# Performance work log

Hardware: AMD Instinct MI355X
Metric: run time of the kernel (lower is better)

The kernel has to match this reference:

```python
import jax, jax.numpy as jnp
import numpy as np

L, B, S, D, H, DK, F = 6, 4, 2048, 512, 8, 64, 2048


def setup_inputs() -> dict:
    key = jax.random.key(0)
    ks = iter(jax.random.split(key, 40))
    def rn(shape, scale=0.02):
        return jax.random.normal(next(ks), shape, jnp.float32) * scale
    inp = {
        "x": jax.random.normal(next(ks), (B, S, D), jnp.float32),
        "enc": jax.random.normal(next(ks), (B, S, D), jnp.float32),
    }
    for pre in ("sa", "ca"):
        inp[f"{pre}_wq"] = rn((L, D, H * DK)); inp[f"{pre}_bq"] = jnp.zeros((L, H * DK), jnp.float32)
        inp[f"{pre}_wk"] = rn((L, D, H * DK)); inp[f"{pre}_bk"] = jnp.zeros((L, H * DK), jnp.float32)
        inp[f"{pre}_wv"] = rn((L, D, H * DK)); inp[f"{pre}_bv"] = jnp.zeros((L, H * DK), jnp.float32)
        inp[f"{pre}_wo"] = rn((L, H * DK, D)); inp[f"{pre}_bo"] = jnp.zeros((L, D), jnp.float32)
    for i in (1, 2, 3):
        inp[f"ln{i}_g"] = jnp.ones((L, D), jnp.float32)
        inp[f"ln{i}_b"] = jnp.zeros((L, D), jnp.float32)
    inp["ff_w1"] = rn((L, D, F)); inp["ff_b1"] = jnp.zeros((L, F), jnp.float32)
    inp["ff_w2"] = rn((L, F, D)); inp["ff_b2"] = jnp.zeros((L, D), jnp.float32)
    return inp


def _layer_norm(z, g, b, eps=1e-5):
    m = z.mean(-1, keepdims=True)
    v = z.var(-1, keepdims=True)
    return (z - m) * jax.lax.rsqrt(v + eps) * g + b


def _mha(q_in, kv_in, wq, bq, wk, bk, wv, bv, wo, bo, causal_bias):
    b, s, _ = q_in.shape
    Q = (q_in @ wq + bq).reshape(b, s, H, DK)   # [B,S,H,DK]
    K = (kv_in @ wk + bk).reshape(b, s, H, DK)
    V = (kv_in @ wv + bv).reshape(b, s, H, DK)
    scores = jnp.einsum("bqhd,bkhd->bhqk", Q, K) / jnp.float32(DK) ** 0.5
    if causal_bias is not None:
        scores = scores + causal_bias  # additive -inf above diagonal
    w = jax.nn.softmax(scores, axis=-1)
    att = jnp.einsum("bhqk,bkhd->bqhd", w, V).reshape(b, s, H * DK)
    return att @ wo + bo


def reference(x, enc, sa_wq, sa_bq, sa_wk, sa_bk, sa_wv, sa_bv, sa_wo, sa_bo,
              ca_wq, ca_bq, ca_wk, ca_bk, ca_wv, ca_bv, ca_wo, ca_bo,
              ln1_g, ln1_b, ln2_g, ln2_b, ln3_g, ln3_b,
              ff_w1, ff_b1, ff_w2, ff_b2):
    s = x.shape[1]
    causal_bias = jnp.triu(jnp.full((s, s), -jnp.inf, jnp.float32), 1)

    params = (sa_wq, sa_bq, sa_wk, sa_bk, sa_wv, sa_bv, sa_wo, sa_bo,
              ca_wq, ca_bq, ca_wk, ca_bk, ca_wv, ca_bv, ca_wo, ca_bo,
              ln1_g, ln1_b, ln2_g, ln2_b, ln3_g, ln3_b,
              ff_w1, ff_b1, ff_w2, ff_b2)

    def block(h, p):
        (swq, sbq, swk, sbk, swv, sbv, swo, sbo,
         cwq, cbq, cwk, cbk, cwv, cbv, cwo, cbo,
         g1, b1, g2, b2, g3, b3, w1, bb1, w2, bb2) = p
        # masked self-attention + residual + LN  (faithful to source)
        x1 = _layer_norm(h + _mha(h, h, swq, sbq, swk, sbk, swv, sbv, swo, sbo, causal_bias), g1, b1)
        # cross-attention; residual comes from the BLOCK INPUT h (source bug kept)
        y = _layer_norm(h + _mha(x1, enc, cwq, cbq, cwk, cbk, cwv, cbv, cwo, cbo, None), g2, b2)
        # FFN; residual from x1 (source bug kept)
        out = _layer_norm(x1 + (jax.nn.relu(y @ w1 + bb1) @ w2 + bb2), g3, b3)
        return out, None

    out, _ = jax.lax.scan(block, x, params)
    return out
```

## Files before the change

kernel.cpp:

```cpp
#include <hip/hip_runtime.h>
#include <stdint.h>

#define LCOUNT 6
#define BB 4
#define SS 2048
#define DD 512
#define HH 8
#define DKK 64
#define FFDIM 2048
#define MM (BB*SS)

typedef __attribute__((ext_vector_type(8))) __bf16 bf16x8;
typedef __attribute__((ext_vector_type(4))) float f32x4;
typedef unsigned short u16;

__device__ __forceinline__ u16 f2bf(float f) {
  union { __bf16 h; u16 u; } v; v.h = (__bf16)f; return v.u;
}
__device__ __forceinline__ float bf2f(u16 u) {
  union { uint32_t u; float f; } v; v.u = ((uint32_t)u) << 16;
  return v.f;
}

__device__ __forceinline__ void gload_lds16(const u16* gsrc, u16* ldst) {
  __builtin_amdgcn_global_load_lds((const __attribute__((address_space(1))) char*)gsrc,
                                   (__attribute__((address_space(3))) char*)ldst, 16, 0, 0);
}

__global__ __launch_bounds__(256)
void prep(const float* __restrict__ x, const float* __restrict__ enc,
          u16* __restrict__ Hb, u16* __restrict__ Eb,
          const float* a0, const float* a1, const float* a2,
          const float* c0, const float* c1, const float* c2,
          float* dqkv, float* dca) {
  if (blockIdx.x < 4096) {
    int i = (blockIdx.x * 256 + threadIdx.x) * 8;
    const int half = MM * 512;
    const float* src = (i < half) ? x : enc;
    u16* dst = (i < half) ? Hb : Eb;
    int j = (i < half) ? i : i - half;
    float4 a = *(const float4*)&src[j];
    float4 b = *(const float4*)&src[j + 4];
    union { u16 us[8]; uint4 v; } pk;
    pk.us[0] = f2bf(a.x); pk.us[1] = f2bf(a.y); pk.us[2] = f2bf(a.z); pk.us[3] = f2bf(a.w);
    pk.us[4] = f2bf(b.x); pk.us[5] = f2bf(b.y); pk.us[6] = f2bf(b.z); pk.us[7] = f2bf(b.w);
    *(uint4*)&dst[j] = pk.v;
  } else {
    int i = (blockIdx.x - 4096) * 256 + threadIdx.x;
    const int half = LCOUNT * 1536;
    if (i >= 2 * half) return;
    bool ca = i >= half;
    int j = ca ? i - half : i;
    int l = j / 1536, cc = j % 1536;
    const float* s = cc < 512 ? (ca ? c0 : a0) : cc < 1024 ? (ca ? c1 : a1) : (ca ? c2 : a2);
    (ca ? dca : dqkv)[j] = s[l * 512 + (cc & 511)];
  }
}

struct WtBatch {
  const float* src[8];
  u16* dst[8];
  unsigned long long lstr[8];
};
__global__ __launch_bounds__(256) void wtrans8(WtBatch wb) {
  __shared__ float tile[64 * 65];
  const int z = blockIdx.z;
  const int slot = z / 6, l = z - slot * 6;
  const float* Wl = wb.src[slot] + (size_t)l * 512 * 512;
  u16* Wtl = wb.dst[slot] + (size_t)l * wb.lstr[slot];
  const int n0 = blockIdx.x * 64, k0 = blockIdx.y * 64;
  const int tid = threadIdx.x;
  const int r = tid >> 2, c4 = (tid & 3) * 16;
#pragma unroll
  for (int j = 0; j < 16; j += 4) {
    float4 v = *(const float4*)&Wl[(size_t)(k0 + r) * 512 + n0 + c4 + j];
    tile[r * 65 + c4 + j + 0] = v.x;
    tile[r * 65 + c4 + j + 1] = v.y;
    tile[r * 65 + c4 + j + 2] = v.z;
    tile[r * 65 + c4 + j + 3] = v.w;
  }
  __syncthreads();
  const int nr = tid >> 2, kc = (tid & 3) * 16;
#pragma unroll
  for (int half = 0; half < 2; ++half) {
    union { u16 us[8]; uint4 v; } pk;
#pragma unroll
    for (int e = 0; e < 8; ++e) pk.us[e] = f2bf(tile[(kc + half * 8 + e) * 65 + nr]);
    *(uint4*)&Wtl[(size_t)(n0 + nr) * 512 + k0 + kc + half * 8] = pk.v;
  }
}

__global__ __launch_bounds__(256)
void wtrans_ffn(const float* __restrict__ w1, const float* __restrict__ w2,
                u16* __restrict__ w1t, u16* __restrict__ w2t) {
  __shared__ float tile[64 * 65];
  const int z = blockIdx.y;
  const bool is2 = z >= 6;
  const int l = is2 ? z - 6 : z;
  const float* Wl = (is2 ? w2 : w1) + (size_t)l * 512 * 2048;
  u16* Wtl = (is2 ? w2t : w1t) + (size_t)l * 512 * 2048;
  const int K_ = is2 ? 2048 : 512, N_ = is2 ? 512 : 2048;
  const int bx = blockIdx.x;
  const int n0 = is2 ? (bx & 7) * 64 : (bx & 31) * 64;
  const int k0 = is2 ? (bx >> 3) * 64 : (bx >> 5) * 64;
  const int tid = threadIdx.x;
  const int r = tid >> 2, c4 = (tid & 3) * 16;
#pragma unroll
  for (int j = 0; j < 16; j += 4) {
    float4 v = *(const float4*)&Wl[(size_t)(k0 + r) * N_ + n0 + c4 + j];
    tile[r * 65 + c4 + j + 0] = v.x;
    tile[r * 65 + c4 + j + 1] = v.y;
    tile[r * 65 + c4 + j + 2] = v.z;
    tile[r * 65 + c4 + j + 3] = v.w;
  }
  __syncthreads();
  const int nr = tid >> 2, kc = (tid & 3) * 16;
#pragma unroll
  for (int half = 0; half < 2; ++half) {
    union { u16 us[8]; uint4 v; } pk;
#pragma unroll
    for (int e = 0; e < 8; ++e) pk.us[e] = f2bf(tile[(kc + half * 8 + e) * 65 + nr]);
    *(uint4*)&Wtl[(size_t)(n0 + nr) * K_ + k0 + kc + half * 8] = pk.v;
  }
}

template <int BMT, int BNT, int BKT, bool RELU, bool VT, bool RES>
__global__ __launch_bounds__(256)
void gemm_bt(const u16* __restrict__ A, const u16* __restrict__ Bt,
             const float* __restrict__ bias, u16* __restrict__ C,
             int N_, int K_, int CS, u16* __restrict__ vt, int vtc0,
             const u16* __restrict__ A2, int a2col,
             const u16* __restrict__ resid) {
  constexpr int MR = BMT / 32;
  constexpr int NR = BNT / 32;
  constexpr int CH = BKT / 8;
  constexpr int RPR = 2048 / BKT;
  constexpr int KS = BKT / 32;
  __shared__ u16 As[BMT * BKT];
  __shared__ u16 Bs[BNT * BKT];
  const int tid = threadIdx.x;
  const int wid = tid >> 6, lane = tid & 63;
  const int l15 = lane & 15, g = lane >> 4;
  const int wr = wid >> 1, wc = wid & 1;
  const int lrow = (CH == 8) ? (lane >> 3) : (lane >> 4);
  const int lch  = lane & (CH - 1);
  const int wrows = 64 / CH;
  const int lin = blockIdx.x + gridDim.x * blockIdx.y;
  const int nwg = gridDim.x * gridDim.y;
  const int swz = (lin & 7) * (nwg >> 3) + (lin >> 3);
  const int brow = (swz / gridDim.x) * BMT;
  const int bcol = (swz % gridDim.x) * BNT;
  const u16* Ap = (A2 != nullptr && bcol >= a2col) ? A2 : A;

  f32x4 acc[MR][NR];
#pragma unroll
  for (int m = 0; m < MR; ++m)
#pragma unroll
    for (int n = 0; n < NR; ++n) acc[m][n] = (f32x4){0.f, 0.f, 0.f, 0.f};

  for (int kt = 0; kt < K_; kt += BKT) {
#pragma unroll
    for (int r = 0; r < BMT / RPR; ++r) {
      int row = r * RPR + wid * wrows + lrow;
      int slot = lch ^ (row & 7);
      gload_lds16(Ap + (size_t)(brow + row) * K_ + kt + slot * 8,
                  &As[r * 2048 + wid * 512]);
    }
#pragma unroll
    for (int r = 0; r < BNT / RPR; ++r) {
      int row = r * RPR + wid * wrows + lrow;
      int slot = lch ^ (row & 7);
      gload_lds16(Bt + (size_t)(bcol + row) * K_ + kt + slot * 8,
                  &Bs[r * 2048 + wid * 512]);
    }
    __syncthreads();
#pragma unroll
    for (int ks = 0; ks < KS; ++ks) {
      bf16x8 af[MR], bfr[NR];
#pragma unroll
      for (int m = 0; m < MR; ++m) {
        int row = wr * (BMT / 2) + m * 16 + l15;
        int slot = (ks * 4 + g) ^ (row & 7);
        af[m] = *(const bf16x8*)&As[row * BKT + slot * 8];
      }
#pragma unroll
      for (int n = 0; n < NR; ++n) {
        int row = wc * (BNT / 2) + n * 16 + l15;
        int slot = (ks * 4 + g) ^ (row & 7);
        bfr[n] = *(const bf16x8*)&Bs[row * BKT + slot * 8];
      }
#pragma unroll
      for (int m = 0; m < MR; ++m)
#pragma unroll
        for (int n = 0; n < NR; ++n)
          acc[m][n] = __builtin_amdgcn_mfma_f32_16x16x32_bf16(af[m], bfr[n], acc[m][n], 0, 0, 0);
    }
    __syncthreads();
  }
#pragma unroll
  for (int n = 0; n < NR; ++n) {
    int col = bcol + wc * (BNT / 2) + n * 16 + l15;
    float bv = bias ? bias[col] : 0.f;
    if (VT && col >= vtc0) {
      int hh = (col - vtc0) >> 6, dd = (col - vtc0) & 63;
#pragma unroll
      for (int m = 0; m < MR; ++m) {
        int s0g = brow + wr * (BMT / 2) + m * 16 + g * 4;
        int bb = s0g >> 11, ss = s0g & (SS - 1);
        union { u16 us[4]; uint2 v; } pk;
#pragma unroll
        for (int r = 0; r < 4; ++r) pk.us[r] = f2bf(acc[m][n][r] + bv);
        *(uint2*)&vt[(((size_t)(bb * HH + hh)) * DKK + dd) * SS + ss] = pk.v;
      }
    } else {
#pragma unroll
      for (int m = 0; m < MR; ++m) {
#pragma unroll
        for (int r = 0; r < 4; ++r) {
          int rowg = brow + wr * (BMT / 2) + m * 16 + g * 4 + r;
          float v = acc[m][n][r] + bv;
          if (RES) v += bf2f(resid[(size_t)rowg * DD + col]);
          if (RELU) v = fmaxf(v, 0.f);
          C[(size_t)rowg * CS + col] = f2bf(v);
        }
      }
    }
  }
}

__global__ __launch_bounds__(256)
void gemm_ln(const u16* __restrict__ A, const u16* __restrict__ Bt,
             const float* __restrict__ bias, const u16* __restrict__ Res,
             const float* __restrict__ gamma, const float* __restrict__ beta,
             u16* __restrict__ Out, float* __restrict__ Ofp, int K_) {
  __shared__ u16 As[16 * 64];
  __shared__ u16 Bs[512 * 64];
  __shared__ float red[4][16][2];
  const int tid = threadIdx.x;
  const int wid = tid >> 6, lane = tid & 63;
  const int l15 = lane & 15, g = lane >> 4;
  const int lin = blockIdx.x;
  const int swz = (lin & 7) * (gridDim.x >> 3) + (lin >> 3);
  const int brow = swz * 16;
  const int lrow8 = lane >> 3, lch = lane & 7;

  f32x4 acc[8];
#pragma unroll
  for (int n = 0; n < 8; ++n) acc[n] = (f32x4){0.f, 0.f, 0.f, 0.f};

  for (int kt = 0; kt < K_; kt += 64) {
#pragma unroll
    for (int r = 0; r < 17; ++r) {
      int u = wid + 4 * r;
      if (u < 66) {
        if (u < 2) {
          int row = u * 8 + lrow8;
          int slot = lch ^ (row & 7);
          gload_lds16(A + (size_t)(brow + row) * K_ + kt + slot * 8, &As[u * 512]);
        } else {
          int row = (u - 2) * 8 + lrow8;
          int slot = lch ^ (row & 7);
          gload_lds16(Bt + (size_t)row * K_ + kt + slot * 8, &Bs[(u - 2) * 512]);
        }
      }
    }
    __syncthreads();
#pragma unroll
    for (int ks = 0; ks < 2; ++ks) {
      bf16x8 af = *(const bf16x8*)&As[l15 * 64 + (((ks * 4 + g) ^ (l15 & 7)) * 8)];
#pragma unroll
      for (int n = 0; n < 8; ++n) {
        int c = wid * 128 + n * 16 + l15;
        bf16x8 bfr = *(const bf16x8*)&Bs[c * 64 + (((ks * 4 + g) ^ (c & 7)) * 8)];
        acc[n] = __builtin_amdgcn_mfma_f32_16x16x32_bf16(af, bfr, acc[n], 0, 0, 0);
      }
    }
    __syncthreads();
  }
#pragma unroll
  for (int rd = 0; rd < 4; ++rd) {
    int off = rd * 2048 + tid * 8;
    int row = off >> 9, col = off & 511;
    uint4 v = *(const uint4*)&Res[(size_t)(brow + row) * DD + col];
    *(uint4*)&Bs[row * 520 + col] = v;
  }
  __syncthreads();
  float z[8][4];
  float s[4] = {0.f, 0.f, 0.f, 0.f}, s2[4] = {0.f, 0.f, 0.f, 0.f};
#pragma unroll
  for (int n = 0; n < 8; ++n) {
    int col = wid * 128 + n * 16 + l15;
    float bv = bias[col];
#pragma unroll
    for (int r = 0; r < 4; ++r) {
      int rl = g * 4 + r;
      float x = acc[n][r] + bv + bf2f(Bs[rl * 520 + col]);
      z[n][r] = x; s[r] += x; s2[r] += x * x;
    }
  }
#pragma unroll
  for (int r = 0; r < 4; ++r) {
    s[r] += __shfl_xor(s[r], 1);  s2[r] += __shfl_xor(s2[r], 1);
    s[r] += __shfl_xor(s[r], 2);  s2[r] += __shfl_xor(s2[r], 2);
    s[r] += __shfl_xor(s[r], 4);  s2[r] += __shfl_xor(s2[r], 4);
    s[r] += __shfl_xor(s[r], 8);  s2[r] += __shfl_xor(s2[r], 8);
  }
  if (l15 == 0) {
#pragma unroll
    for (int r = 0; r < 4; ++r) {
      red[wid][g * 4 + r][0] = s[r];
      red[wid][g * 4 + r][1] = s2[r];
    }
  }
  __syncthreads();
  float mean[4], rs[4];
#pragma unroll
  for (int r = 0; r < 4; ++r) {
    int rl = g * 4 + r;
    float ts  = red[0][rl][0] + red[1][rl][0] + red[2][rl][0] + red[3][rl][0];
    float ts2 = red[0][rl][1] + red[1][rl][1] + red[2][rl][1] + red[3][rl][1];
    float mn = ts * (1.f / 512.f);
    float var = ts2 * (1.f / 512.f) - mn * mn;
    mean[r] = mn; rs[r] = rsqrtf(var + 1e-5f);
  }
#pragma unroll
  for (int n = 0; n < 8; ++n) {
    int col = wid * 128 + n * 16 + l15;
    float gm = gamma[col], bt = beta[col];
#pragma unroll
    for (int r = 0; r < 4; ++r) {
      int rowg = brow + g * 4 + r;
      float o = (z[n][r] - mean[r]) * rs[r] * gm + bt;
      Out[(size_t)rowg * DD + col] = f2bf(o);
      if (Ofp) Ofp[(size_t)rowg * DD + col] = o;
    }
  }
}

__global__ __launch_bounds__(256)
void ln_kernel(const u16* __restrict__ A,
               const float* __restrict__ gamma, const float* __restrict__ beta,
               u16* __restrict__ out_bf, float* __restrict__ out_f32) {
  const int row = blockIdx.x * 4 + (threadIdx.x >> 6);
  const int lane = threadIdx.x & 63;
  uint4 av = *(const uint4*)&A[(size_t)row * DD + lane * 8];
  const u16* au = (const u16*)&av;
  float z[8], s = 0.f, s2 = 0.f;
#pragma unroll
  for (int j = 0; j < 8; ++j) {
    float x = bf2f(au[j]);
    z[j] = x; s += x; s2 += x * x;
  }
#pragma unroll
  for (int off = 1; off < 64; off <<= 1) {
    s += __shfl_xor(s, off);
    s2 += __shfl_xor(s2, off);
  }
  float mean = s * (1.f / 512.f);
  float var = s2 * (1.f / 512.f) - mean * mean;
  float rs = rsqrtf(var + 1e-5f);
  union { u16 us[8]; uint4 v; } pk;
#pragma unroll
  for (int j = 0; j < 8; ++j) {
    float o = (z[j] - mean) * rs * gamma[lane * 8 + j] + beta[lane * 8 + j];
    pk.us[j] = f2bf(o);
    if (out_f32) out_f32[(size_t)row * DD + lane * 8 + j] = o;
  }
  *(uint4*)&out_bf[(size_t)row * DD + lane * 8] = pk.v;
}

template <bool CAUSAL>
__global__ __launch_bounds__(256, 4)
void attn_kernel(const u16* __restrict__ Qm, const u16* __restrict__ Km,
                 const u16* __restrict__ Vt, u16* __restrict__ Om, int qks) {
  __shared__ u16 Ks[2][64 * 64];
  __shared__ u16 Vs[2][64 * 64];
  __shared__ u16 Ps[4][16 * 64];
  const int lin = blockIdx.x;
  const int bh = (lin & 7) * 4 + ((lin >> 3) >> 5);
  const int qc = (lin >> 3) & 31;
  const int qb = (qc & 1) ? (31 - (qc >> 1)) : (qc >> 1);
  const int h = bh & 7, b = bh >> 3;
  const int tid = threadIdx.x, wid = tid >> 6, lane = tid & 63;
  const int l15 = lane & 15, g = lane >> 4;
  const int qstart = qb * 64;
  const size_t qbase = ((size_t)b * SS) * qks + h * DKK;
  const size_t vtbase = (size_t)(b * HH + h) * DKK * SS;
  const size_t obase = ((size_t)b * SS) * DD + h * DKK;
  u16* psw = &Ps[wid][0];
  const int srow = wid * 8 + (lane >> 3);
  const int sslot = lane & 7;
  const int qg = qstart + wid * 16 + l15;
  const int pswz = (l15 & 7) << 1;
  const float SC = 0.18033688f;

  const u16* kp = Km + qbase;
  const u16* vp = Vt + vtbase;

  bf16x8 qf[2];
#pragma unroll
  for (int ks = 0; ks < 2; ++ks)
    qf[ks] = *(const bf16x8*)&Qm[qbase + (size_t)qg * qks + ks * 32 + g * 8];

  f32x4 oacc[4];
#pragma unroll
  for (int nb = 0; nb < 4; ++nb) oacc[nb] = (f32x4){0.f, 0.f, 0.f, 0.f};
  float m_run = -3.0e38f, l_run = 0.f;

  const int T = CAUSAL ? (qb + 1) : (SS / 64);

#pragma unroll
  for (int r = 0; r < 2; ++r) {
    int row = r * 32 + srow;
    int slot = sslot ^ (row & 7);
    gload_lds16(kp + (size_t)row * qks + slot * 8, &Ks[0][r * 2048 + wid * 512]);
    gload_lds16(vp + (size_t)row * SS + slot * 8, &Vs[0][r * 2048 + wid * 512]);
  }
  __syncthreads();

  int cur = 0;
  for (int t = 0; t < T; ++t) {
    const int kstart = t * 64;
    if (t + 1 < T) {
#pragma unroll
      for (int r = 0; r < 2; ++r) {
        int row = r * 32 + srow;
        int slot = sslot ^ (row & 7);
        gload_lds16(kp + (size_t)(kstart + 64 + row) * qks + slot * 8,
                    &Ks[cur ^ 1][r * 2048 + wid * 512]);
        gload_lds16(vp + (size_t)row * SS + kstart + 64 + slot * 8,
                    &Vs[cur ^ 1][r * 2048 + wid * 512]);
      }
    }
    f32x4 sacc[4];
#pragma unroll
    for (int nb = 0; nb < 4; ++nb) sacc[nb] = (f32x4){0.f, 0.f, 0.f, 0.f};
    __builtin_amdgcn_s_setprio(1);
#pragma unroll
    for (int nb = 0; nb < 4; ++nb) {
      int row = nb * 16 + l15;
#pragma unroll
      for (int ks = 0; ks < 2; ++ks) {
        bf16x8 kf = *(const bf16x8*)&Ks[cur][row * 64 + (((ks * 4 + g) ^ (row & 7)) * 8)];
        sacc[nb] = __builtin_amdgcn_mfma_f32_16x16x32_bf16(kf, qf[ks], sacc[nb], 0, 0, 0);
      }
    }
    __builtin_amdgcn_s_setprio(0);
    if (CAUSAL && t == T - 1) {
#pragma unroll
      for (int nb = 0; nb < 4; ++nb)
#pragma unroll
        for (int r = 0; r < 4; ++r)
          if ((kstart + nb * 16 + g * 4 + r) > qg) sacc[nb][r] = -3.0e38f;
    }
    f32x4 m4 = sacc[0];
#pragma unroll
    for (int nb = 1; nb < 4; ++nb) {
      m4[0] = fmaxf(m4[0], sacc[nb][0]); m4[1] = fmaxf(m4[1], sacc[nb][1]);
      m4[2] = fmaxf(m4[2], sacc[nb][2]); m4[3] = fmaxf(m4[3], sacc[nb][3]);
    }
    float mx = fmaxf(fmaxf(m4[0], m4[1]), fmaxf(m4[2], m4[3]));
    mx = fmaxf(mx, __shfl_xor(mx, 16));
    mx = fmaxf(mx, __shfl_xor(mx, 32));
    const bool skip = __all(mx <= m_run + 64.0f);
    float mnew = skip ? m_run : fmaxf(m_run, mx);
    float mc = mnew * SC;
    float s = 0.f;
#pragma unroll
    for (int nb = 0; nb < 4; ++nb) {
#pragma unroll
      for (int r = 0; r < 4; ++r) {
        float e = __builtin_amdgcn_exp2f(sacc[nb][r] * SC - mc);
        sacc[nb][r] = e; s += e;
      }
    }
    s += __shfl_xor(s, 16);
    s += __shfl_xor(s, 32);
    if (skip) {
      l_run += s;
    } else {
      float resc = __builtin_amdgcn_exp2f((m_run - mnew) * SC);
      l_run = l_run * resc + s;
      m_run = mnew;
      float ro[4];
#pragma unroll
      for (int r = 0; r < 4; ++r) ro[r] = __shfl(resc, g * 4 + r);
#pragma unroll
      for (int nb = 0; nb < 4; ++nb)
#pragma unroll
        for (int r = 0; r < 4; ++r) oacc[nb][r] *= ro[r];
    }
#pragma unroll
    for (int nb = 0; nb < 4; ++nb) {
      union { u16 us[4]; uint2 v; } pk;
#pragma unroll
      for (int r = 0; r < 4; ++r) pk.us[r] = f2bf(sacc[nb][r]);
      int cp = (nb * 4 + g) ^ pswz;
      *(uint2*)&psw[l15 * 64 + cp * 4] = pk.v;
    }
    bf16x8 pf[2];
#pragma unroll
    for (int ks = 0; ks < 2; ++ks) {
      int cp0 = (8 * ks + 2 * g) ^ pswz;
      pf[ks] = *(const bf16x8*)&psw[l15 * 64 + cp0 * 4];
    }
    __builtin_amdgcn_s_setprio(1);
#pragma unroll
    for (int nb = 0; nb < 4; ++nb) {
      int row = nb * 16 + l15;
#pragma unroll
      for (int ks = 0; ks < 2; ++ks) {
        bf16x8 vf = *(const bf16x8*)&Vs[cur][row * 64 + (((ks * 4 + g) ^ (row & 7)) * 8)];
        oacc[nb] = __builtin_amdgcn_mfma_f32_16x16x32_bf16(pf[ks], vf, oacc[nb], 0, 0, 0);
      }
    }
    __builtin_amdgcn_s_setprio(0);
    __syncthreads();
    cur ^= 1;
  }
  float linv = 1.f / l_run;
  float io[4];
#pragma unroll
  for (int r = 0; r < 4; ++r) io[r] = __shfl(linv, g * 4 + r);
#pragma unroll
  for (int nb = 0; nb < 4; ++nb) {
#pragma unroll
    for (int r = 0; r < 4; ++r) {
      Om[obase + (size_t)(qstart + wid * 16 + g * 4 + r) * DD + nb * 16 + l15] =
          f2bf(oacc[nb][r] * io[r]);
    }
  }
}

extern "C" void kernel_launch(void* const* d_in, const int* in_sizes, int n_in,
                              void* d_out, int out_size, void* d_ws, size_t ws_size,
                              hipStream_t stream) {
  const float* x   = (const float*)d_in[0];
  const float* enc = (const float*)d_in[1];
  const float* sa_w[4] = {(const float*)d_in[2], (const float*)d_in[4], (const float*)d_in[6], (const float*)d_in[8]};
  const float* sa_b[4] = {(const float*)d_in[3], (const float*)d_in[5], (const float*)d_in[7], (const float*)d_in[9]};
  const float* ca_w[4] = {(const float*)d_in[10], (const float*)d_in[12], (const float*)d_in[14], (const float*)d_in[16]};
  const float* ca_b[4] = {(const float*)d_in[11], (const float*)d_in[13], (const float*)d_in[15], (const float*)d_in[17]};
  const float* ln_g[3] = {(const float*)d_in[18], (const float*)d_in[20], (const float*)d_in[22]};
  const float* ln_b[3] = {(const float*)d_in[19], (const float*)d_in[21], (const float*)d_in[23]};
  const float* ffw1 = (const float*)d_in[24];
  const float* ffb1 = (const float*)d_in[25];
  const float* ffw2 = (const float*)d_in[26];
  const float* ffb2 = (const float*)d_in[27];

  char* ws = (char*)d_ws;
  size_t o = 0;
  auto take = [&](size_t bytes) {
    void* p = ws + o;
    o += (bytes + 255) & ~(size_t)255;
    return p;
  };
  u16* wqkv  = (u16*)take((size_t)LCOUNT * 1536 * 512 * 2);
  u16* wca   = (u16*)take((size_t)LCOUNT * 1536 * 512 * 2);
  u16* wosa  = (u16*)take((size_t)LCOUNT * 512 * 512 * 2);
  u16* woca  = (u16*)take((size_t)LCOUNT * 512 * 512 * 2);
  u16* w1t   = (u16*)take((size_t)LCOUNT * 512 * 2048 * 2);
  u16* w2t   = (u16*)take((size_t)LCOUNT * 2048 * 512 * 2);
  float* bqkv = (float*)take((size_t)LCOUNT * 1536 * 4);
  float* bca  = (float*)take((size_t)LCOUNT * 1536 * 4);
  u16* Hb   = (u16*)take((size_t)MM * 512 * 2);
  u16* Eb   = (u16*)take((size_t)MM * 512 * 2);
  u16* QKVb = (u16*)take((size_t)MM * 1536 * 2);
  u16* Ab   = (u16*)take((size_t)MM * 512 * 2);
  u16* Pb   = (u16*)take((size_t)MM * 512 * 2);
  u16* X1b  = (u16*)take((size_t)MM * 512 * 2);
  u16* Yb   = (u16*)take((size_t)MM * 512 * 2);
  u16* Fb   = (u16*)take((size_t)MM * 2048 * 2);
  u16* Vtb  = Fb;

  prep<<<4168, 256, 0, stream>>>(x, enc, Hb, Eb,
                                 sa_b[0], sa_b[1], sa_b[2],
                                 ca_b[0], ca_b[1], ca_b[2], bqkv, bca);
  WtBatch wb;
  wb.src[0] = sa_w[0]; wb.dst[0] = wqkv;              wb.lstr[0] = (size_t)1536 * 512;
  wb.src[1] = sa_w[1]; wb.dst[1] = wqkv + 512 * 512;  wb.lstr[1] = (size_t)1536 * 512;
  wb.src[2] = sa_w[2]; wb.dst[2] = wqkv + 1024 * 512; wb.lstr[2] = (size_t)1536 * 512;
  wb.src[3] = sa_w[3]; wb.dst[3] = wosa;              wb.lstr[3] = (size_t)512 * 512;
  wb.src[4] = ca_w[0]; wb.dst[4] = wca;               wb.lstr[4] = (size_t)1536 * 512;
  wb.src[5] = ca_w[1]; wb.dst[5] = wca + 512 * 512;   wb.lstr[5] = (size_t)1536 * 512;
  wb.src[6] = ca_w[2]; wb.dst[6] = wca + 1024 * 512;  wb.lstr[6] = (size_t)1536 * 512;
  wb.src[7] = ca_w[3]; wb.dst[7] = woca;              wb.lstr[7] = (size_t)512 * 512;
  wtrans8<<<dim3(8, 8, 48), 256, 0, stream>>>(wb);
  wtrans_ffn<<<dim3(256, 12), 256, 0, stream>>>(ffw1, ffw2, w1t, w2t);

  for (int l = 0; l < LCOUNT; ++l) {
    const size_t w512 = (size_t)l * 512 * 512;
    const size_t wff = (size_t)l * 512 * 2048;
    gemm_bt<128, 128, 64, false, true, false><<<dim3(12, 64), 256, 0, stream>>>(
        Hb, wqkv + (size_t)l * 1536 * 512, bqkv + l * 1536, QKVb, 1536, 512, 1536, Vtb, 1024,
        nullptr, 0, nullptr);
    attn_kernel<true><<<dim3(1024), 256, 0, stream>>>(QKVb, QKVb + 512, Vtb, Ab, 1536);
    gemm_ln<<<dim3(512), 256, 0, stream>>>(Ab, wosa + w512, sa_b[3] + l * 512, Hb,
                                           ln_g[0] + l * 512, ln_b[0] + l * 512,
                                           X1b, nullptr, 512);
    gemm_bt<128, 128, 64, false, true, false><<<dim3(12, 64), 256, 0, stream>>>(
        X1b, wca + (size_t)l * 1536 * 512, bca + l * 1536, QKVb, 1536, 512, 1536, Vtb, 1024,
        Eb, 512, nullptr);
    attn_kernel<false><<<dim3(1024), 256, 0, stream>>>(QKVb, QKVb + 512, Vtb, Ab, 1536);
    gemm_ln<<<dim3(512), 256, 0, stream>>>(Ab, woca + w512, ca_b[3] + l * 512, Hb,
                                           ln_g[1] + l * 512, ln_b[1] + l * 512,
                                           Yb, nullptr, 512);
    gemm_bt<128, 128, 64, true, false, false><<<dim3(16, 64), 256, 0, stream>>>(
        Yb, w1t + wff, ffb1 + l * 2048, Fb, 2048, 512, 2048, nullptr, 0, nullptr, 0, nullptr);
    gemm_bt<64, 128, 128, false, false, true><<<dim3(4, 128), 256, 0, stream>>>(
        Fb, w2t + wff, ffb2 + l * 512, Pb, 512, 2048, 512, nullptr, 0, nullptr, 0, X1b);
    ln_kernel<<<MM / 4, 256, 0, stream>>>(Pb, ln_g[2] + l * 512, ln_b[2] + l * 512, Hb,
                                          (l == LCOUNT - 1) ? (float*)d_out : nullptr);
  }
}
```

Before: 1.720 ms.

## Load K/V tiles directly from global into registers in attention kernel

Attention no longer stages K and V tiles in double-buffered shared memory. Each wave loads its MFMA fragments straight from global memory into registers, prefetching the next K tile into registers and reloading V every iteration. This removes the LDS traffic and the per-iteration block barrier. In exchange, all four waves redundantly fetch the same K/V data from global/L2, register pressure goes up, and the occupancy hint in launch bounds is dropped.

```diff
diff --git a/kernel.cpp b/kernel.cpp
--- a/kernel.cpp
+++ b/kernel.cpp
@@ -370,11 +370,9 @@
 }
 
 template <bool CAUSAL>
-__global__ __launch_bounds__(256, 4)
+__global__ __launch_bounds__(256)
 void attn_kernel(const u16* __restrict__ Qm, const u16* __restrict__ Km,
                  const u16* __restrict__ Vt, u16* __restrict__ Om, int qks) {
-  __shared__ u16 Ks[2][64 * 64];
-  __shared__ u16 Vs[2][64 * 64];
   __shared__ u16 Ps[4][16 * 64];
   const int lin = blockIdx.x;
   const int bh = (lin & 7) * 4 + ((lin >> 3) >> 5);
@@ -388,19 +386,18 @@
   const size_t vtbase = (size_t)(b * HH + h) * DKK * SS;
   const size_t obase = ((size_t)b * SS) * DD + h * DKK;
   u16* psw = &Ps[wid][0];
-  const int srow = wid * 8 + (lane >> 3);
-  const int sslot = lane & 7;
   const int qg = qstart + wid * 16 + l15;
   const int pswz = (l15 & 7) << 1;
   const float SC = 0.18033688f;
 
   const u16* kp = Km + qbase;
   const u16* vp = Vt + vtbase;
+  const int gcol = g * 8;
 
   bf16x8 qf[2];
 #pragma unroll
   for (int ks = 0; ks < 2; ++ks)
-    qf[ks] = *(const bf16x8*)&Qm[qbase + (size_t)qg * qks + ks * 32 + g * 8];
+    qf[ks] = *(const bf16x8*)&Qm[qbase + (size_t)qg * qks + ks * 32 + gcol];
 
   f32x4 oacc[4];
 #pragma unroll
@@ -409,42 +406,38 @@
 
   const int T = CAUSAL ? (qb + 1) : (SS / 64);
 
-#pragma unroll
-  for (int r = 0; r < 2; ++r) {
-    int row = r * 32 + srow;
-    int slot = sslot ^ (row & 7);
-    gload_lds16(kp + (size_t)row * qks + slot * 8, &Ks[0][r * 2048 + wid * 512]);
-    gload_lds16(vp + (size_t)row * SS + slot * 8, &Vs[0][r * 2048 + wid * 512]);
-  }
-  __syncthreads();
-
-  int cur = 0;
+  bf16x8 kc[8], kn[8], vc[8];
+#pragma unroll
+  for (int nb = 0; nb < 4; ++nb)
+#pragma unroll
+    for (int ks = 0; ks < 2; ++ks)
+      kc[nb * 2 + ks] = *(const bf16x8*)&kp[(size_t)(nb * 16 + l15) * qks + ks * 32 + gcol];
+
   for (int t = 0; t < T; ++t) {
     const int kstart = t * 64;
+#pragma unroll
+    for (int nb = 0; nb < 4; ++nb)
+#pragma unroll
+      for (int ks = 0; ks < 2; ++ks)
+        vc[nb * 2 + ks] =
+            *(const bf16x8*)&vp[(size_t)(nb * 16 + l15) * SS + kstart + ks * 32 + gcol];
     if (t + 1 < T) {
 #pragma unroll
-      for (int r = 0; r < 2; ++r) {
-        int row = r * 32 + srow;
-        int slot = sslot ^ (row & 7);
-        gload_lds16(kp + (size_t)(kstart + 64 + row) * qks + slot * 8,
-                    &Ks[cur ^ 1][r * 2048 + wid * 512]);
-        gload_lds16(vp + (size_t)row * SS + kstart + 64 + slot * 8,
-                    &Vs[cur ^ 1][r * 2048 + wid * 512]);
-      }
+      for (int nb = 0; nb < 4; ++nb)
+#pragma unroll
+        for (int ks = 0; ks < 2; ++ks)
+          kn[nb * 2 + ks] =
+              *(const bf16x8*)&kp[(size_t)(kstart + 64 + nb * 16 + l15) * qks + ks * 32 + gcol];
     }
     f32x4 sacc[4];
 #pragma unroll
     for (int nb = 0; nb < 4; ++nb) sacc[nb] = (f32x4){0.f, 0.f, 0.f, 0.f};
     __builtin_amdgcn_s_setprio(1);
 #pragma unroll
-    for (int nb = 0; nb < 4; ++nb) {
-      int row = nb * 16 + l15;
-#pragma unroll
-      for (int ks = 0; ks < 2; ++ks) {
-        bf16x8 kf = *(const bf16x8*)&Ks[cur][row * 64 + (((ks * 4 + g) ^ (row & 7)) * 8)];
-        sacc[nb] = __builtin_amdgcn_mfma_f32_16x16x32_bf16(kf, qf[ks], sacc[nb], 0, 0, 0);
-      }
-    }
+    for (int nb = 0; nb < 4; ++nb)
+#pragma unroll
+      for (int ks = 0; ks < 2; ++ks)
+        sacc[nb] = __builtin_amdgcn_mfma_f32_16x16x32_bf16(kc[nb * 2 + ks], qf[ks], sacc[nb], 0, 0, 0);
     __builtin_amdgcn_s_setprio(0);
     if (CAUSAL && t == T - 1) {
 #pragma unroll
@@ -506,17 +499,15 @@
     }
     __builtin_amdgcn_s_setprio(1);
 #pragma unroll
-    for (int nb = 0; nb < 4; ++nb) {
-      int row = nb * 16 + l15;
-#pragma unroll
-      for (int ks = 0; ks < 2; ++ks) {
-        bf16x8 vf = *(const bf16x8*)&Vs[cur][row * 64 + (((ks * 4 + g) ^ (row & 7)) * 8)];
-        oacc[nb] = __builtin_amdgcn_mfma_f32_16x16x32_bf16(pf[ks], vf, oacc[nb], 0, 0, 0);
-      }
-    }
+    for (int nb = 0; nb < 4; ++nb)
+#pragma unroll
+      for (int ks = 0; ks < 2; ++ks)
+        oacc[nb] = __builtin_amdgcn_mfma_f32_16x16x32_bf16(pf[ks], vc[nb * 2 + ks], oacc[nb], 0, 0, 0);
     __builtin_amdgcn_s_setprio(0);
-    __syncthreads();
-    cur ^= 1;
+    if (t + 1 < T) {
+#pragma unroll
+      for (int i = 0; i < 8; ++i) kc[i] = kn[i];
+    }
   }
   float linv = 1.f / l_run;
   float io[4];
```

Result: slower. 3.562 ms (+107.1%).
